# Performance work log

Measured on AMD Instinct MI355X. Metric: run time of the kernel, lower is better.

## Reference

```python
import jax, jax.numpy as jnp
import numpy as np
import math

HIDDEN = 1024
NUM_HEADS = 16
HEAD_DIM = HIDDEN // NUM_HEADS


def _rope_tables(seq_len, dim, dtype):
    inv_freq = 1.0 / (10000.0 ** (np.arange(0, dim, 2, dtype=np.float32) / dim))
    t = np.arange(seq_len, dtype=np.float32)
    freqs = np.einsum('i,j->ij', t, inv_freq)          # [S, dim/2]
    emb = np.concatenate([freqs, freqs], axis=-1)      # [S, dim]
    return jnp.asarray(np.cos(emb), dtype), jnp.asarray(np.sin(emb), dtype)


def _rotate_half(x):
    x1, x2 = x[..., : x.shape[-1] // 2], x[..., x.shape[-1] // 2:]
    return jnp.concatenate([-x2, x1], axis=-1)


def setup_inputs() -> dict:
    key = jax.random.key(0)
    k1, k2, k3 = jax.random.split(key, 3)
    B, S = 2, 2048
    x = jax.random.normal(k1, (B, S, HIDDEN), dtype=jnp.float32)
    attention_mask = jnp.ones((B, S), dtype=jnp.int32)
    w_qkv = jax.random.normal(k2, (HIDDEN, 3 * HIDDEN), dtype=jnp.float32) * (1.0 / math.sqrt(HIDDEN))
    w_out = jax.random.normal(k3, (HIDDEN, HIDDEN), dtype=jnp.float32) * (1.0 / math.sqrt(HIDDEN))
    return {"x": x, "attention_mask": attention_mask, "w_qkv": w_qkv, "w_out": w_out}


def reference(x, attention_mask, w_qkv, w_out):
    B, S, H = x.shape
    qkv = x @ w_qkv                                   # [B,S,3H]
    qkv = qkv.reshape(B, S, NUM_HEADS, 3 * HEAD_DIM).transpose(0, 2, 1, 3)  # [B,h,S,3d]
    q, k, v = jnp.split(qkv, 3, axis=-1)              # each [B,h,S,d]
    cos, sin = _rope_tables(S, HEAD_DIM, x.dtype)     # [S,d]
    cos = cos[None, None]
    sin = sin[None, None]
    q = q * cos + _rotate_half(q) * sin
    k = k * cos + _rotate_half(k) * sin
    scale = math.sqrt(HEAD_DIM)
    scores = jnp.einsum('bhqd,bhkd->bhqk', q, k) / scale  # [B,h,S,S]
    mask_value = jnp.finfo(scores.dtype).min
    scores = jnp.where(attention_mask[:, None, None, :] == 0, mask_value, scores)
    attn = jax.nn.softmax(scores, axis=-1)
    context = jnp.einsum('bhqk,bhkd->bhqd', attn, v)  # [B,h,S,d]
    context = context.transpose(0, 2, 1, 3).reshape(B, S, H)
    return context @ w_out
```

## Files before the change

### kernel.cpp

```cpp
#include <hip/hip_runtime.h>
#include <hip/hip_bf16.h>
#include <math.h>
#include <stdint.h>


typedef __bf16 bf16;
typedef __bf16 bf16x8 __attribute__((ext_vector_type(8)));
typedef __bf16 bf16x4 __attribute__((ext_vector_type(4)));
typedef float f32x4 __attribute__((ext_vector_type(4)));

#define AS1 __attribute__((address_space(1)))
#define AS3 __attribute__((address_space(3)))

__device__ __forceinline__ void gload_lds16(const void* g, void* l) {
  __builtin_amdgcn_global_load_lds((const AS1 void*)g, (AS3 void*)l, 16, 0, 0);
}

__device__ __forceinline__ f32x4 mfma16(bf16x8 a, bf16x8 b, f32x4 c) {
  return __builtin_amdgcn_mfma_f32_16x16x32_bf16(a, b, c, 0, 0, 0);
}

#define S_LEN 2048


__global__ void k_split_x(const float* __restrict__ x, bf16* __restrict__ xh,
                          bf16* __restrict__ xl) {
  int i = blockIdx.x * 256 + threadIdx.x;
  float4 v = ((const float4*)x)[i];
  float vv[4] = {v.x, v.y, v.z, v.w};
  bf16x4 h, l;
#pragma unroll
  for (int j = 0; j < 4; j++) {
    bf16 hb = (bf16)vv[j];
    h[j] = hb;
    l[j] = (bf16)(vv[j] - (float)hb);
  }
  ((bf16x4*)xh)[i] = h;
  ((bf16x4*)xl)[i] = l;
}

__global__ void k_wt_qkv(const float* __restrict__ w, bf16* __restrict__ bth,
                         bf16* __restrict__ btl) {
  __shared__ float t[32][33];
  int n0 = blockIdx.x * 32, k0 = blockIdx.y * 32;
  int tx = threadIdx.x & 31, ty = threadIdx.x >> 5;
#pragma unroll
  for (int i = 0; i < 4; i++)
    t[ty + 8 * i][tx] = w[(size_t)(k0 + ty + 8 * i) * 3072 + n0 + tx];
  __syncthreads();
#pragma unroll
  for (int i = 0; i < 4; i++) {
    int r = ty + 8 * i;
    float v = t[tx][r];
    size_t o = (size_t)(n0 + r) * 1024 + k0 + tx;
    bf16 hb = (bf16)v;
    bth[o] = hb;
    btl[o] = (bf16)(v - (float)hb);
  }
}

__global__ void k_wt_out(const float* __restrict__ w, bf16* __restrict__ bt) {
  __shared__ float t[32][33];
  int n0 = blockIdx.x * 32, k0 = blockIdx.y * 32;
  int tx = threadIdx.x & 31, ty = threadIdx.x >> 5;
#pragma unroll
  for (int i = 0; i < 4; i++)
    t[ty + 8 * i][tx] = w[(size_t)(k0 + ty + 8 * i) * 1024 + n0 + tx];
  __syncthreads();
#pragma unroll
  for (int i = 0; i < 4; i++) {
    int r = ty + 8 * i;
    bt[(size_t)(n0 + r) * 1024 + k0 + tx] = (bf16)t[tx][r];
  }
}

__global__ void k_rope_tables(float* __restrict__ ct, float* __restrict__ st) {
  int i = blockIdx.x * 256 + threadIdx.x;
  int s = i >> 5, j = i & 31;
  double invf = pow(10000.0, -(double)j / 32.0);
  double a = (double)s * invf;
  ct[i] = (float)cos(a);
  st[i] = (float)sin(a);
}

__global__ __launch_bounds__(256, 2) void k_gemm_qkv(
    const bf16* __restrict__ Ah, const bf16* __restrict__ Al,
    const bf16* __restrict__ Bh, const bf16* __restrict__ Bl,
    bf16* __restrict__ C) {
  const int K = 1024, N = 3072;
  __shared__ __align__(16) bf16 sAh[128 * 32];
  __shared__ __align__(16) bf16 sAl[128 * 32];
  __shared__ __align__(16) bf16 sBh[128 * 32];
  __shared__ __align__(16) bf16 sBl[128 * 32];
  int tid = threadIdx.x, lane = tid & 63, wid = tid >> 6;
  int m0 = blockIdx.x * 128, n0 = blockIdx.y * 128;
  int wm = wid >> 1, wn = wid & 1;

  f32x4 acc[4][4];
#pragma unroll
  for (int a = 0; a < 4; a++)
#pragma unroll
    for (int b = 0; b < 4; b++) acc[a][b] = (f32x4){0.f, 0.f, 0.f, 0.f};

  for (int k0 = 0; k0 < K; k0 += 32) {
#pragma unroll
    for (int p = 0; p < 2; p++) {
      int slot = p * 256 + tid;
      int row = slot >> 2, c16 = slot & 3;
      int cs = c16 ^ ((row >> 1) & 3);
      int ldsoff = (p * 256 + wid * 64) * 16;
      size_t ga = (size_t)(m0 + row) * K + k0 + cs * 8;
      size_t gb = (size_t)(n0 + row) * K + k0 + cs * 8;
      gload_lds16(Ah + ga, (char*)sAh + ldsoff);
      gload_lds16(Al + ga, (char*)sAl + ldsoff);
      gload_lds16(Bh + gb, (char*)sBh + ldsoff);
      gload_lds16(Bl + gb, (char*)sBl + ldsoff);
    }
    __syncthreads();

    bf16x8 fah[4], fal[4], fbh[4], fbl[4];
#pragma unroll
    for (int mf = 0; mf < 4; mf++) {
      int row = wm * 64 + mf * 16 + (lane & 15);
      int c16 = (lane >> 4) ^ ((row >> 1) & 3);
      int off = row * 64 + c16 * 16;
      fah[mf] = *(const bf16x8*)((const char*)sAh + off);
      fal[mf] = *(const bf16x8*)((const char*)sAl + off);
    }
#pragma unroll
    for (int nf = 0; nf < 4; nf++) {
      int row = wn * 64 + nf * 16 + (lane & 15);
      int c16 = (lane >> 4) ^ ((row >> 1) & 3);
      int off = row * 64 + c16 * 16;
      fbh[nf] = *(const bf16x8*)((const char*)sBh + off);
      fbl[nf] = *(const bf16x8*)((const char*)sBl + off);
    }
#pragma unroll
    for (int mf = 0; mf < 4; mf++)
#pragma unroll
      for (int nf = 0; nf < 4; nf++) {
        acc[mf][nf] = mfma16(fah[mf], fbh[nf], acc[mf][nf]);
        acc[mf][nf] = mfma16(fah[mf], fbl[nf], acc[mf][nf]);
        acc[mf][nf] = mfma16(fal[mf], fbh[nf], acc[mf][nf]);
      }
    __syncthreads();
  }

#pragma unroll
  for (int mf = 0; mf < 4; mf++)
#pragma unroll
    for (int nf = 0; nf < 4; nf++)
#pragma unroll
      for (int r = 0; r < 4; r++) {
        int row = m0 + wm * 64 + mf * 16 + (lane >> 4) * 4 + r;
        int col = n0 + wn * 64 + nf * 16 + (lane & 15);
        C[(size_t)row * N + col] = (bf16)acc[mf][nf][r];
      }
}

__global__ void k_rope_scatter(const bf16* __restrict__ QKV,
                               const float* __restrict__ ct,
                               const float* __restrict__ st,
                               bf16* __restrict__ Q, bf16* __restrict__ Kb,
                               bf16* __restrict__ Vt) {
  __shared__ __align__(16) bf16 vt[64 * 64];
  int sblk = blockIdx.x, bh = blockIdx.y;
  int b = bh >> 4, h = bh & 15;
  int tid = threadIdx.x;
  int r = tid >> 2, c = tid & 3;
  int s = sblk * 64 + r;
  size_t rowbase = ((size_t)(b * S_LEN + s)) * 3072 + h * 192;

  bf16x8 qlo = *(const bf16x8*)(QKV + rowbase + c * 8);
  bf16x8 qhi = *(const bf16x8*)(QKV + rowbase + c * 8 + 32);
  bf16x8 klo = *(const bf16x8*)(QKV + rowbase + 64 + c * 8);
  bf16x8 khi = *(const bf16x8*)(QKV + rowbase + 64 + c * 8 + 32);
  bf16x8 vlo = *(const bf16x8*)(QKV + rowbase + 128 + c * 8);
  bf16x8 vhi = *(const bf16x8*)(QKV + rowbase + 128 + c * 8 + 32);

  bf16x8 qol, qoh, kol, koh;
#pragma unroll
  for (int j = 0; j < 8; j++) {
    float cs = ct[s * 32 + c * 8 + j], sn = st[s * 32 + c * 8 + j];
    float q1 = (float)qlo[j], q2 = (float)qhi[j];
    qol[j] = (bf16)(q1 * cs - q2 * sn);
    qoh[j] = (bf16)(q2 * cs + q1 * sn);
    float k1 = (float)klo[j], k2 = (float)khi[j];
    kol[j] = (bf16)(k1 * cs - k2 * sn);
    koh[j] = (bf16)(k2 * cs + k1 * sn);
  }
  size_t qb = ((size_t)bh * S_LEN + s) * 64 + c * 8;
  *(bf16x8*)(Q + qb) = qol;
  *(bf16x8*)(Q + qb + 32) = qoh;
  *(bf16x8*)(Kb + qb) = kol;
  *(bf16x8*)(Kb + qb + 32) = koh;

#pragma unroll
  for (int j = 0; j < 8; j++) {
    vt[(c * 8 + j) * 64 + r] = vlo[j];
    vt[(c * 8 + 32 + j) * 64 + r] = vhi[j];
  }
  __syncthreads();
  int d = tid >> 2, cc = tid & 3;
  size_t vb = ((size_t)bh * 64 + d) * S_LEN + sblk * 64 + cc * 16;
  *(bf16x8*)(Vt + vb) = *(const bf16x8*)(vt + d * 64 + cc * 16);
  *(bf16x8*)(Vt + vb + 8) = *(const bf16x8*)(vt + d * 64 + cc * 16 + 8);
}

__global__ __launch_bounds__(256, 3) void k_attn(
    const bf16* __restrict__ Q, const bf16* __restrict__ Kb,
    const bf16* __restrict__ Vt, const int* __restrict__ mask,
    bf16* __restrict__ Ctx) {
  __shared__ __align__(16) bf16 sK[128 * 64];
  __shared__ __align__(16) bf16 sV[64 * 128];
  int tid = threadIdx.x, lane = tid & 63, wid = tid >> 6;
  int g = lane >> 4, q = lane & 15;
  int qt = blockIdx.x, bh = blockIdx.y;
  int b = bh >> 4, h = bh & 15;
  int q0 = qt * 128 + wid * 32;

  bf16x8 bQ[2][2];
#pragma unroll
  for (int mf = 0; mf < 2; mf++)
#pragma unroll
    for (int ks = 0; ks < 2; ks++) {
      const bf16* p = Q + ((size_t)bh * S_LEN + q0 + mf * 16 + q) * 64 + ks * 32 + g * 8;
      bf16x8 v = *(const bf16x8*)p;
#pragma unroll
      for (int j = 0; j < 8; j++) v[j] = (bf16)((float)v[j] * 0.125f);
      bQ[mf][ks] = v;
    }

  f32x4 O[2][4];
  float mrow[2], lrow[2];
#pragma unroll
  for (int mf = 0; mf < 2; mf++) {
#pragma unroll
    for (int nd = 0; nd < 4; nd++) O[mf][nd] = (f32x4){0.f, 0.f, 0.f, 0.f};
    mrow[mf] = -3e38f;
    lrow[mf] = 0.f;
  }

  for (int kt = 0; kt < 16; kt++) {
    int k0 = kt * 128;
#pragma unroll
    for (int p = 0; p < 4; p++) {
      int slot = p * 256 + tid;
      int row = slot >> 3, c16 = slot & 7;
      int cs = c16 ^ (row & 7);
      gload_lds16(Kb + ((size_t)bh * S_LEN + k0 + row) * 64 + cs * 8,
                  (char*)sK + (p * 256 + wid * 64) * 16);
    }
#pragma unroll
    for (int p = 0; p < 4; p++) {
      int slot = p * 256 + tid;
      int row = slot >> 4, c16 = slot & 15;
      int cs = c16 ^ (row & 7);
      gload_lds16(Vt + ((size_t)bh * 64 + row) * S_LEN + k0 + cs * 8,
                  (char*)sV + (p * 256 + wid * 64) * 16);
    }
    __syncthreads();

    f32x4 sfr[2][8];
#pragma unroll
    for (int mf = 0; mf < 2; mf++)
#pragma unroll
      for (int kf = 0; kf < 8; kf++) sfr[mf][kf] = (f32x4){0.f, 0.f, 0.f, 0.f};
#pragma unroll
    for (int kf = 0; kf < 8; kf++) {
#pragma unroll
      for (int ks = 0; ks < 2; ks++) {
        int row = kf * 16 + q;
        int c16 = (ks * 4 + g) ^ (row & 7);
        bf16x8 ak = *(const bf16x8*)((const char*)sK + row * 128 + c16 * 16);
        sfr[0][kf] = mfma16(ak, bQ[0][ks], sfr[0][kf]);
        sfr[1][kf] = mfma16(ak, bQ[1][ks], sfr[1][kf]);
      }
    }
#pragma unroll
    for (int kf = 0; kf < 8; kf++) {
      int4 mv = *(const int4*)(mask + b * S_LEN + k0 + kf * 16 + g * 4);
      int mm[4] = {mv.x, mv.y, mv.z, mv.w};
#pragma unroll
      for (int r = 0; r < 4; r++)
        if (mm[r] == 0) { sfr[0][kf][r] = -1e30f; sfr[1][kf][r] = -1e30f; }
    }
    float alpha[2];
#pragma unroll
    for (int mf = 0; mf < 2; mf++) {
      float mx = -3e38f;
#pragma unroll
      for (int kf = 0; kf < 8; kf++)
#pragma unroll
        for (int r = 0; r < 4; r++) mx = fmaxf(mx, sfr[mf][kf][r]);
      mx = fmaxf(mx, __shfl_xor(mx, 16, 64));
      mx = fmaxf(mx, __shfl_xor(mx, 32, 64));
      float mnew = fmaxf(mrow[mf], mx);
      float al = __expf(mrow[mf] - mnew);
      mrow[mf] = mnew;
      float ps = 0.f;
#pragma unroll
      for (int kf = 0; kf < 8; kf++)
#pragma unroll
        for (int r = 0; r < 4; r++) {
          float p0 = __expf(sfr[mf][kf][r] - mnew);
          sfr[mf][kf][r] = p0;
          ps += p0;
        }
      ps += __shfl_xor(ps, 16, 64);
      ps += __shfl_xor(ps, 32, 64);
      lrow[mf] = lrow[mf] * al + ps;
      alpha[mf] = al;
    }
#pragma unroll
    for (int mf = 0; mf < 2; mf++)
#pragma unroll
      for (int nd = 0; nd < 4; nd++)
#pragma unroll
        for (int r = 0; r < 4; r++) O[mf][nd][r] *= alpha[mf];

#pragma unroll
    for (int ks = 0; ks < 4; ks++) {
      bf16x8 pb[2];
#pragma unroll
      for (int mf = 0; mf < 2; mf++)
#pragma unroll
        for (int j = 0; j < 8; j++)
          pb[mf][j] = (bf16)sfr[mf][2 * ks + (j >> 2)][j & 3];
#pragma unroll
      for (int nd = 0; nd < 4; nd++) {
        int row = nd * 16 + q;
        int sw = (row & 7) << 4;
        bf16x4 v0 = *(const bf16x4*)((const char*)sV + row * 256 + ((ks * 64 + g * 8) ^ sw));
        bf16x4 v1 = *(const bf16x4*)((const char*)sV + row * 256 + ((ks * 64 + g * 8 + 32) ^ sw));
        bf16x8 av;
#pragma unroll
        for (int j = 0; j < 4; j++) { av[j] = v0[j]; av[4 + j] = v1[j]; }
#pragma unroll
        for (int mf = 0; mf < 2; mf++) O[mf][nd] = mfma16(av, pb[mf], O[mf][nd]);
      }
    }
    __syncthreads();
  }

#pragma unroll
  for (int mf = 0; mf < 2; mf++) {
    float inv = 1.f / lrow[mf];
    int srow = q0 + mf * 16 + q;
#pragma unroll
    for (int nd = 0; nd < 4; nd++) {
      bf16x4 o4;
#pragma unroll
      for (int r = 0; r < 4; r++) o4[r] = (bf16)(O[mf][nd][r] * inv);
      *(bf16x4*)(Ctx + ((size_t)b * S_LEN + srow) * 1024 + h * 64 + nd * 16 + g * 4) = o4;
    }
  }
}

__global__ __launch_bounds__(256, 2) void k_gemm_out(
    const bf16* __restrict__ A, const bf16* __restrict__ Bt,
    float* __restrict__ C) {
  const int K = 1024, N = 1024;
  __shared__ __align__(16) bf16 sA[128 * 32];
  __shared__ __align__(16) bf16 sB[128 * 32];
  int tid = threadIdx.x, lane = tid & 63, wid = tid >> 6;
  int m0 = blockIdx.x * 128, n0 = blockIdx.y * 128;
  int wm = wid >> 1, wn = wid & 1;

  f32x4 acc[4][4];
#pragma unroll
  for (int a = 0; a < 4; a++)
#pragma unroll
    for (int b = 0; b < 4; b++) acc[a][b] = (f32x4){0.f, 0.f, 0.f, 0.f};

  for (int k0 = 0; k0 < K; k0 += 32) {
#pragma unroll
    for (int p = 0; p < 2; p++) {
      int slot = p * 256 + tid;
      int row = slot >> 2, c16 = slot & 3;
      int cs = c16 ^ ((row >> 1) & 3);
      int ldsoff = (p * 256 + wid * 64) * 16;
      gload_lds16(A + (size_t)(m0 + row) * K + k0 + cs * 8, (char*)sA + ldsoff);
      gload_lds16(Bt + (size_t)(n0 + row) * K + k0 + cs * 8, (char*)sB + ldsoff);
    }
    __syncthreads();
    bf16x8 fa[4], fb[4];
#pragma unroll
    for (int mf = 0; mf < 4; mf++) {
      int row = wm * 64 + mf * 16 + (lane & 15);
      int c16 = (lane >> 4) ^ ((row >> 1) & 3);
      fa[mf] = *(const bf16x8*)((const char*)sA + row * 64 + c16 * 16);
    }
#pragma unroll
    for (int nf = 0; nf < 4; nf++) {
      int row = wn * 64 + nf * 16 + (lane & 15);
      int c16 = (lane >> 4) ^ ((row >> 1) & 3);
      fb[nf] = *(const bf16x8*)((const char*)sB + row * 64 + c16 * 16);
    }
#pragma unroll
    for (int mf = 0; mf < 4; mf++)
#pragma unroll
      for (int nf = 0; nf < 4; nf++)
        acc[mf][nf] = mfma16(fa[mf], fb[nf], acc[mf][nf]);
    __syncthreads();
  }
#pragma unroll
  for (int mf = 0; mf < 4; mf++)
#pragma unroll
    for (int nf = 0; nf < 4; nf++)
#pragma unroll
      for (int r = 0; r < 4; r++) {
        int row = m0 + wm * 64 + mf * 16 + (lane >> 4) * 4 + r;
        int col = n0 + wn * 64 + nf * 16 + (lane & 15);
        C[(size_t)row * N + col] = acc[mf][nf][r];
      }
}

extern "C" void kernel_launch(void* const* d_in, const int* in_sizes, int n_in,
                              void* d_out, int out_size, void* d_ws, size_t ws_size,
                              hipStream_t stream) {
  const float* x = (const float*)d_in[0];
  const int* mask = (const int*)d_in[1];
  const float* wqkv = (const float*)d_in[2];
  const float* wout = (const float*)d_in[3];
  float* out = (float*)d_out;
  char* ws = (char*)d_ws;

  bf16* Xh  = (bf16*)(ws + 0);
  bf16* Xl  = (bf16*)(ws + 8388608);
  bf16* Wqh = (bf16*)(ws + 16777216);
  bf16* Wql = (bf16*)(ws + 23068672);
  bf16* Wo  = (bf16*)(ws + 29360128);
  bf16* QKV = (bf16*)(ws + 31457280);
  bf16* Qb  = (bf16*)(ws + 56623104);
  bf16* Kb  = (bf16*)(ws + 65011712);
  bf16* Vt  = (bf16*)(ws + 73400320);
  bf16* Ctx = (bf16*)(ws + 81788928);
  float* ct = (float*)(ws + 90177536);
  float* st = (float*)(ws + 90439680);

  k_split_x<<<4096, 256, 0, stream>>>(x, Xh, Xl);
  k_wt_qkv<<<dim3(96, 32), 256, 0, stream>>>(wqkv, Wqh, Wql);
  k_wt_out<<<dim3(32, 32), 256, 0, stream>>>(wout, Wo);
  k_rope_tables<<<256, 256, 0, stream>>>(ct, st);
  k_gemm_qkv<<<dim3(32, 24), 256, 0, stream>>>(Xh, Xl, Wqh, Wql, QKV);
  k_rope_scatter<<<dim3(32, 32), 256, 0, stream>>>(QKV, ct, st, Qb, Kb, Vt);
  k_attn<<<dim3(16, 32), 256, 0, stream>>>(Qb, Kb, Vt, mask, Ctx);
  k_gemm_out<<<dim3(32, 8), 256, 0, stream>>>(Ctx, Wo, out);
}
```

Before: 265.3 us.

## Split attention keys across two wave groups with double-buffered K and merge

The attention kernel now runs 512 threads per block. Two groups of four waves each handle half of the key range, and their partial softmax states are merged through LDS at the end (split-K flash attention). K tiles are double-buffered in LDS, V is read straight from global memory instead of staged, and Q is prescaled by log2(e)/sqrt(d) in the rope kernel so exp2 can replace exp. It also skips the mask pass when a whole tile is unmasked and skips output rescaling unless the running max grows by more than 8 (lazy rescale). In exchange, V reads from global may be less coalesced, and the 64KB LDS arena limits occupancy.

```diff
diff --git a/kernel.cpp b/kernel.cpp
--- a/kernel.cpp
+++ b/kernel.cpp
@@ -21,6 +21,7 @@
 }
 
 #define S_LEN 2048
+#define QSCALE 0.1803368801111144f
 
 
 __global__ void k_split_x(const float* __restrict__ x, bf16* __restrict__ xh,
@@ -183,8 +184,8 @@
   for (int j = 0; j < 8; j++) {
     float cs = ct[s * 32 + c * 8 + j], sn = st[s * 32 + c * 8 + j];
     float q1 = (float)qlo[j], q2 = (float)qhi[j];
-    qol[j] = (bf16)(q1 * cs - q2 * sn);
-    qoh[j] = (bf16)(q2 * cs + q1 * sn);
+    qol[j] = (bf16)((q1 * cs - q2 * sn) * QSCALE);
+    qoh[j] = (bf16)((q2 * cs + q1 * sn) * QSCALE);
     float k1 = (float)klo[j], k2 = (float)khi[j];
     kol[j] = (bf16)(k1 * cs - k2 * sn);
     koh[j] = (bf16)(k2 * cs + k1 * sn);
@@ -207,29 +208,25 @@
   *(bf16x8*)(Vt + vb + 8) = *(const bf16x8*)(vt + d * 64 + cc * 16 + 8);
 }
 
-__global__ __launch_bounds__(256, 3) void k_attn(
+__global__ __launch_bounds__(512, 4) void k_attn(
     const bf16* __restrict__ Q, const bf16* __restrict__ Kb,
     const bf16* __restrict__ Vt, const int* __restrict__ mask,
     bf16* __restrict__ Ctx) {
-  __shared__ __align__(16) bf16 sK[128 * 64];
-  __shared__ __align__(16) bf16 sV[64 * 128];
-  int tid = threadIdx.x, lane = tid & 63, wid = tid >> 6;
+  __shared__ __align__(16) char arena[65536];
+  int tid = threadIdx.x, lane = tid & 63, w = tid >> 6;
+  int grp = w >> 2, wq = w & 3;
   int g = lane >> 4, q = lane & 15;
   int qt = blockIdx.x, bh = blockIdx.y;
   int b = bh >> 4, h = bh & 15;
-  int q0 = qt * 128 + wid * 32;
+  int q0 = qt * 128 + wq * 32;
 
   bf16x8 bQ[2][2];
 #pragma unroll
   for (int mf = 0; mf < 2; mf++)
 #pragma unroll
-    for (int ks = 0; ks < 2; ks++) {
-      const bf16* p = Q + ((size_t)bh * S_LEN + q0 + mf * 16 + q) * 64 + ks * 32 + g * 8;
-      bf16x8 v = *(const bf16x8*)p;
-#pragma unroll
-      for (int j = 0; j < 8; j++) v[j] = (bf16)((float)v[j] * 0.125f);
-      bQ[mf][ks] = v;
-    }
+    for (int ks = 0; ks < 2; ks++)
+      bQ[mf][ks] = *(const bf16x8*)(Q + ((size_t)bh * S_LEN + q0 + mf * 16 + q) * 64 +
+                                    ks * 32 + g * 8);
 
   f32x4 O[2][4];
   float mrow[2], lrow[2];
@@ -241,25 +238,35 @@
     lrow[mf] = 0.f;
   }
 
-  for (int kt = 0; kt < 16; kt++) {
-    int k0 = kt * 128;
-#pragma unroll
-    for (int p = 0; p < 4; p++) {
-      int slot = p * 256 + tid;
-      int row = slot >> 3, c16 = slot & 7;
-      int cs = c16 ^ (row & 7);
-      gload_lds16(Kb + ((size_t)bh * S_LEN + k0 + row) * 64 + cs * 8,
-                  (char*)sK + (p * 256 + wid * 64) * 16);
-    }
-#pragma unroll
-    for (int p = 0; p < 4; p++) {
-      int slot = p * 256 + tid;
-      int row = slot >> 4, c16 = slot & 15;
-      int cs = c16 ^ (row & 7);
-      gload_lds16(Vt + ((size_t)bh * 64 + row) * S_LEN + k0 + cs * 8,
-                  (char*)sV + (p * 256 + wid * 64) * 16);
-    }
-    __syncthreads();
+  const bf16* kbase = Kb + (size_t)bh * S_LEN * 64;
+  const bf16* vbase = Vt + (size_t)bh * 64 * S_LEN;
+  int db = 0;
+
+#pragma unroll
+  for (int p = 0; p < 4; p++) {
+    int slot = p * 512 + tid;
+    int sg = slot >> 10, within = slot & 1023;
+    int row = within >> 3, c16 = within & 7;
+    int cs = c16 ^ (row & 7);
+    gload_lds16(kbase + (size_t)(sg * 1024 + row) * 64 + cs * 8,
+                arena + slot * 16);
+  }
+  __syncthreads();
+
+  for (int kt = 0; kt < 8; kt++) {
+    int k0 = grp * 1024 + kt * 128;
+    if (kt < 7) {
+#pragma unroll
+      for (int p = 0; p < 4; p++) {
+        int slot = p * 512 + tid;
+        int sg = slot >> 10, within = slot & 1023;
+        int row = within >> 3, c16 = within & 7;
+        int cs = c16 ^ (row & 7);
+        gload_lds16(kbase + (size_t)(sg * 1024 + (kt + 1) * 128 + row) * 64 + cs * 8,
+                    arena + (db ^ 1) * 32768 + slot * 16);
+      }
+    }
+    const char* kt_lds = arena + db * 32768 + grp * 16384;
 
     f32x4 sfr[2][8];
 #pragma unroll
@@ -272,20 +279,24 @@
       for (int ks = 0; ks < 2; ks++) {
         int row = kf * 16 + q;
         int c16 = (ks * 4 + g) ^ (row & 7);
-        bf16x8 ak = *(const bf16x8*)((const char*)sK + row * 128 + c16 * 16);
+        bf16x8 ak = *(const bf16x8*)(kt_lds + row * 128 + c16 * 16);
         sfr[0][kf] = mfma16(ak, bQ[0][ks], sfr[0][kf]);
         sfr[1][kf] = mfma16(ak, bQ[1][ks], sfr[1][kf]);
       }
     }
-#pragma unroll
-    for (int kf = 0; kf < 8; kf++) {
-      int4 mv = *(const int4*)(mask + b * S_LEN + k0 + kf * 16 + g * 4);
-      int mm[4] = {mv.x, mv.y, mv.z, mv.w};
-#pragma unroll
-      for (int r = 0; r < 4; r++)
-        if (mm[r] == 0) { sfr[0][kf][r] = -1e30f; sfr[1][kf][r] = -1e30f; }
-    }
-    float alpha[2];
+    {
+      int2 mv = *(const int2*)(mask + b * S_LEN + k0 + lane * 2);
+      if (!__all(mv.x & mv.y)) {
+#pragma unroll
+        for (int kf = 0; kf < 8; kf++) {
+          int4 m4 = *(const int4*)(mask + b * S_LEN + k0 + kf * 16 + g * 4);
+          int mm[4] = {m4.x, m4.y, m4.z, m4.w};
+#pragma unroll
+          for (int r = 0; r < 4; r++)
+            if (mm[r] == 0) { sfr[0][kf][r] = -1e30f; sfr[1][kf][r] = -1e30f; }
+        }
+      }
+    }
 #pragma unroll
     for (int mf = 0; mf < 2; mf++) {
       float mx = -3e38f;
@@ -295,29 +306,29 @@
         for (int r = 0; r < 4; r++) mx = fmaxf(mx, sfr[mf][kf][r]);
       mx = fmaxf(mx, __shfl_xor(mx, 16, 64));
       mx = fmaxf(mx, __shfl_xor(mx, 32, 64));
-      float mnew = fmaxf(mrow[mf], mx);
-      float al = __expf(mrow[mf] - mnew);
-      mrow[mf] = mnew;
+      if (__any(mx > mrow[mf] + 8.0f)) {
+        float mnew = fmaxf(mrow[mf], mx);
+        float al = exp2f(mrow[mf] - mnew);
+        mrow[mf] = mnew;
+        lrow[mf] *= al;
+#pragma unroll
+        for (int nd = 0; nd < 4; nd++)
+#pragma unroll
+          for (int r = 0; r < 4; r++) O[mf][nd][r] *= al;
+      }
       float ps = 0.f;
 #pragma unroll
       for (int kf = 0; kf < 8; kf++)
 #pragma unroll
         for (int r = 0; r < 4; r++) {
-          float p0 = __expf(sfr[mf][kf][r] - mnew);
+          float p0 = exp2f(sfr[mf][kf][r] - mrow[mf]);
           sfr[mf][kf][r] = p0;
           ps += p0;
         }
       ps += __shfl_xor(ps, 16, 64);
       ps += __shfl_xor(ps, 32, 64);
-      lrow[mf] = lrow[mf] * al + ps;
-      alpha[mf] = al;
-    }
-#pragma unroll
-    for (int mf = 0; mf < 2; mf++)
-#pragma unroll
-      for (int nd = 0; nd < 4; nd++)
-#pragma unroll
-        for (int r = 0; r < 4; r++) O[mf][nd][r] *= alpha[mf];
+      lrow[mf] += ps;
+    }
 
 #pragma unroll
     for (int ks = 0; ks < 4; ks++) {
@@ -329,10 +340,9 @@
           pb[mf][j] = (bf16)sfr[mf][2 * ks + (j >> 2)][j & 3];
 #pragma unroll
       for (int nd = 0; nd < 4; nd++) {
-        int row = nd * 16 + q;
-        int sw = (row & 7) << 4;
-        bf16x4 v0 = *(const bf16x4*)((const char*)sV + row * 256 + ((ks * 64 + g * 8) ^ sw));
-        bf16x4 v1 = *(const bf16x4*)((const char*)sV + row * 256 + ((ks * 64 + g * 8 + 32) ^ sw));
+        const bf16* vrow = vbase + (size_t)(nd * 16 + q) * S_LEN + k0 + ks * 32;
+        bf16x4 v0 = *(const bf16x4*)(vrow + g * 4);
+        bf16x4 v1 = *(const bf16x4*)(vrow + 16 + g * 4);
         bf16x8 av;
 #pragma unroll
         for (int j = 0; j < 4; j++) { av[j] = v0[j]; av[4 + j] = v1[j]; }
@@ -341,18 +351,43 @@
       }
     }
     __syncthreads();
-  }
-
-#pragma unroll
-  for (int mf = 0; mf < 2; mf++) {
-    float inv = 1.f / lrow[mf];
-    int srow = q0 + mf * 16 + q;
-#pragma unroll
-    for (int nd = 0; nd < 4; nd++) {
-      bf16x4 o4;
-#pragma unroll
-      for (int r = 0; r < 4; r++) o4[r] = (bf16)(O[mf][nd][r] * inv);
-      *(bf16x4*)(Ctx + ((size_t)b * S_LEN + srow) * 1024 + h * 64 + nd * 16 + g * 4) = o4;
+    db ^= 1;
+  }
+
+  float* mO = (float*)arena;
+  float2* mML = (float2*)(arena + 33280);
+  if (grp == 1) {
+#pragma unroll
+    for (int mf = 0; mf < 2; mf++) {
+      int row = wq * 32 + mf * 16 + q;
+      if (g == 0) mML[row] = make_float2(mrow[mf], lrow[mf]);
+#pragma unroll
+      for (int nd = 0; nd < 4; nd++)
+#pragma unroll
+        for (int r = 0; r < 4; r++)
+          mO[row * 65 + nd * 16 + g * 4 + r] = O[mf][nd][r];
+    }
+  }
+  __syncthreads();
+  if (grp == 0) {
+#pragma unroll
+    for (int mf = 0; mf < 2; mf++) {
+      int row = wq * 32 + mf * 16 + q;
+      float2 ml2 = mML[row];
+      float m = fmaxf(mrow[mf], ml2.x);
+      float fA = exp2f(mrow[mf] - m), fB = exp2f(ml2.x - m);
+      float inv = 1.f / (lrow[mf] * fA + ml2.y * fB);
+      int srow = q0 + mf * 16 + q;
+#pragma unroll
+      for (int nd = 0; nd < 4; nd++) {
+        bf16x4 o4;
+#pragma unroll
+        for (int r = 0; r < 4; r++) {
+          float ob = mO[row * 65 + nd * 16 + g * 4 + r];
+          o4[r] = (bf16)((O[mf][nd][r] * fA + ob * fB) * inv);
+        }
+        *(bf16x4*)(Ctx + ((size_t)b * S_LEN + srow) * 1024 + h * 64 + nd * 16 + g * 4) = o4;
+      }
     }
   }
 }
@@ -445,6 +480,6 @@
   k_rope_tables<<<256, 256, 0, stream>>>(ct, st);
   k_gemm_qkv<<<dim3(32, 24), 256, 0, stream>>>(Xh, Xl, Wqh, Wql, QKV);
   k_rope_scatter<<<dim3(32, 32), 256, 0, stream>>>(QKV, ct, st, Qb, Kb, Vt);
-  k_attn<<<dim3(16, 32), 256, 0, stream>>>(Qb, Kb, Vt, mask, Ctx);
+  k_attn<<<dim3(16, 32), 512, 0, stream>>>(Qb, Kb, Vt, mask, Ctx);
   k_gemm_out<<<dim3(32, 8), 256, 0, stream>>>(Ctx, Wo, out);
 }
```

Result: slower. 370.6 us (+39.7%).

## Restructure attention kernel: double-buffered K, direct V reads, lazy rescale, exp2

Applied to the files above, without the earlier changes.

The attention kernel now gives each wave 16 query rows instead of 32 and launches twice as many blocks, ordered by head first. K tiles are double-buffered in LDS so the next tile's load overlaps compute, while V is read straight from global memory rather than staged in LDS. The softmax scale and log2(e) are folded into Q during the RoPE pass so exp2f can be used. Output rescaling is skipped unless the running max rises by more than 8, and mask handling is skipped when a wave sees no masked keys. Reading V from global memory avoids the LDS staging but may raise L2 traffic, and each K tile loaded into LDS is now shared by only 64 query rows instead of 128.

```diff
diff --git a/kernel.cpp b/kernel.cpp
--- a/kernel.cpp
+++ b/kernel.cpp
@@ -21,6 +21,7 @@
 }
 
 #define S_LEN 2048
+#define QSCALE 0.1803368801111144f
 
 
 __global__ void k_split_x(const float* __restrict__ x, bf16* __restrict__ xh,
@@ -183,8 +184,8 @@
   for (int j = 0; j < 8; j++) {
     float cs = ct[s * 32 + c * 8 + j], sn = st[s * 32 + c * 8 + j];
     float q1 = (float)qlo[j], q2 = (float)qhi[j];
-    qol[j] = (bf16)(q1 * cs - q2 * sn);
-    qoh[j] = (bf16)(q2 * cs + q1 * sn);
+    qol[j] = (bf16)((q1 * cs - q2 * sn) * QSCALE);
+    qoh[j] = (bf16)((q2 * cs + q1 * sn) * QSCALE);
     float k1 = (float)klo[j], k2 = (float)khi[j];
     kol[j] = (bf16)(k1 * cs - k2 * sn);
     koh[j] = (bf16)(k2 * cs + k1 * sn);
@@ -207,153 +208,141 @@
   *(bf16x8*)(Vt + vb + 8) = *(const bf16x8*)(vt + d * 64 + cc * 16 + 8);
 }
 
-__global__ __launch_bounds__(256, 3) void k_attn(
+__global__ __launch_bounds__(256, 4) void k_attn(
     const bf16* __restrict__ Q, const bf16* __restrict__ Kb,
     const bf16* __restrict__ Vt, const int* __restrict__ mask,
     bf16* __restrict__ Ctx) {
-  __shared__ __align__(16) bf16 sK[128 * 64];
-  __shared__ __align__(16) bf16 sV[64 * 128];
-  int tid = threadIdx.x, lane = tid & 63, wid = tid >> 6;
+  __shared__ __align__(16) char sK[2][16384];
+  int tid = threadIdx.x, lane = tid & 63, w = tid >> 6;
   int g = lane >> 4, q = lane & 15;
-  int qt = blockIdx.x, bh = blockIdx.y;
+  int bh = blockIdx.x, qt = blockIdx.y;
   int b = bh >> 4, h = bh & 15;
-  int q0 = qt * 128 + wid * 32;
-
-  bf16x8 bQ[2][2];
-#pragma unroll
-  for (int mf = 0; mf < 2; mf++)
-#pragma unroll
-    for (int ks = 0; ks < 2; ks++) {
-      const bf16* p = Q + ((size_t)bh * S_LEN + q0 + mf * 16 + q) * 64 + ks * 32 + g * 8;
-      bf16x8 v = *(const bf16x8*)p;
-#pragma unroll
-      for (int j = 0; j < 8; j++) v[j] = (bf16)((float)v[j] * 0.125f);
-      bQ[mf][ks] = v;
-    }
-
-  f32x4 O[2][4];
-  float mrow[2], lrow[2];
-#pragma unroll
-  for (int mf = 0; mf < 2; mf++) {
-#pragma unroll
-    for (int nd = 0; nd < 4; nd++) O[mf][nd] = (f32x4){0.f, 0.f, 0.f, 0.f};
-    mrow[mf] = -3e38f;
-    lrow[mf] = 0.f;
-  }
+  int qrow = qt * 64 + w * 16 + q;
+
+  bf16x8 bQ[2];
+#pragma unroll
+  for (int ks = 0; ks < 2; ks++)
+    bQ[ks] = *(const bf16x8*)(Q + ((size_t)bh * S_LEN + qrow) * 64 + ks * 32 + g * 8);
+
+  f32x4 O[4];
+#pragma unroll
+  for (int nd = 0; nd < 4; nd++) O[nd] = (f32x4){0.f, 0.f, 0.f, 0.f};
+  float mrow = -3e38f, lrow = 0.f;
+
+  const bf16* kbase = Kb + (size_t)bh * S_LEN * 64;
+  const bf16* vbase = Vt + (size_t)bh * 64 * S_LEN;
+  int db = 0;
+
+#pragma unroll
+  for (int p = 0; p < 4; p++) {
+    int slot = p * 256 + tid;
+    int row = slot >> 3, c16 = slot & 7;
+    int cs = c16 ^ (row & 7);
+    gload_lds16(kbase + (size_t)row * 64 + cs * 8,
+                sK[0] + (p * 256 + w * 64) * 16);
+  }
+  __syncthreads();
 
   for (int kt = 0; kt < 16; kt++) {
     int k0 = kt * 128;
-#pragma unroll
-    for (int p = 0; p < 4; p++) {
-      int slot = p * 256 + tid;
-      int row = slot >> 3, c16 = slot & 7;
-      int cs = c16 ^ (row & 7);
-      gload_lds16(Kb + ((size_t)bh * S_LEN + k0 + row) * 64 + cs * 8,
-                  (char*)sK + (p * 256 + wid * 64) * 16);
-    }
-#pragma unroll
-    for (int p = 0; p < 4; p++) {
-      int slot = p * 256 + tid;
-      int row = slot >> 4, c16 = slot & 15;
-      int cs = c16 ^ (row & 7);
-      gload_lds16(Vt + ((size_t)bh * 64 + row) * S_LEN + k0 + cs * 8,
-                  (char*)sV + (p * 256 + wid * 64) * 16);
-    }
-    __syncthreads();
-
-    f32x4 sfr[2][8];
-#pragma unroll
-    for (int mf = 0; mf < 2; mf++)
-#pragma unroll
-      for (int kf = 0; kf < 8; kf++) sfr[mf][kf] = (f32x4){0.f, 0.f, 0.f, 0.f};
+    if (kt < 15) {
+#pragma unroll
+      for (int p = 0; p < 4; p++) {
+        int slot = p * 256 + tid;
+        int row = slot >> 3, c16 = slot & 7;
+        int cs = c16 ^ (row & 7);
+        gload_lds16(kbase + (size_t)((kt + 1) * 128 + row) * 64 + cs * 8,
+                    sK[db ^ 1] + (p * 256 + w * 64) * 16);
+      }
+    }
+    const char* kl = sK[db];
+
+    f32x4 sfr[8];
+#pragma unroll
+    for (int kf = 0; kf < 8; kf++) sfr[kf] = (f32x4){0.f, 0.f, 0.f, 0.f};
 #pragma unroll
     for (int kf = 0; kf < 8; kf++) {
 #pragma unroll
       for (int ks = 0; ks < 2; ks++) {
         int row = kf * 16 + q;
         int c16 = (ks * 4 + g) ^ (row & 7);
-        bf16x8 ak = *(const bf16x8*)((const char*)sK + row * 128 + c16 * 16);
-        sfr[0][kf] = mfma16(ak, bQ[0][ks], sfr[0][kf]);
-        sfr[1][kf] = mfma16(ak, bQ[1][ks], sfr[1][kf]);
-      }
-    }
-#pragma unroll
-    for (int kf = 0; kf < 8; kf++) {
-      int4 mv = *(const int4*)(mask + b * S_LEN + k0 + kf * 16 + g * 4);
-      int mm[4] = {mv.x, mv.y, mv.z, mv.w};
-#pragma unroll
-      for (int r = 0; r < 4; r++)
-        if (mm[r] == 0) { sfr[0][kf][r] = -1e30f; sfr[1][kf][r] = -1e30f; }
-    }
-    float alpha[2];
-#pragma unroll
-    for (int mf = 0; mf < 2; mf++) {
+        bf16x8 ak = *(const bf16x8*)(kl + row * 128 + c16 * 16);
+        sfr[kf] = mfma16(ak, bQ[ks], sfr[kf]);
+      }
+    }
+    {
+      int2 mv = *(const int2*)(mask + b * S_LEN + k0 + lane * 2);
+      if (!__all(mv.x & mv.y)) {
+#pragma unroll
+        for (int kf = 0; kf < 8; kf++) {
+          int4 m4 = *(const int4*)(mask + b * S_LEN + k0 + kf * 16 + g * 4);
+          int mm[4] = {m4.x, m4.y, m4.z, m4.w};
+#pragma unroll
+          for (int r = 0; r < 4; r++)
+            if (mm[r] == 0) sfr[kf][r] = -1e30f;
+        }
+      }
+    }
+    {
       float mx = -3e38f;
 #pragma unroll
       for (int kf = 0; kf < 8; kf++)
 #pragma unroll
-        for (int r = 0; r < 4; r++) mx = fmaxf(mx, sfr[mf][kf][r]);
+        for (int r = 0; r < 4; r++) mx = fmaxf(mx, sfr[kf][r]);
       mx = fmaxf(mx, __shfl_xor(mx, 16, 64));
       mx = fmaxf(mx, __shfl_xor(mx, 32, 64));
-      float mnew = fmaxf(mrow[mf], mx);
-      float al = __expf(mrow[mf] - mnew);
-      mrow[mf] = mnew;
+      if (__any(mx > mrow + 8.0f)) {
+        float mnew = fmaxf(mrow, mx);
+        float al = exp2f(mrow - mnew);
+        mrow = mnew;
+        lrow *= al;
+#pragma unroll
+        for (int nd = 0; nd < 4; nd++)
+#pragma unroll
+          for (int r = 0; r < 4; r++) O[nd][r] *= al;
+      }
       float ps = 0.f;
 #pragma unroll
       for (int kf = 0; kf < 8; kf++)
 #pragma unroll
         for (int r = 0; r < 4; r++) {
-          float p0 = __expf(sfr[mf][kf][r] - mnew);
-          sfr[mf][kf][r] = p0;
+          float p0 = exp2f(sfr[kf][r] - mrow);
+          sfr[kf][r] = p0;
           ps += p0;
         }
       ps += __shfl_xor(ps, 16, 64);
       ps += __shfl_xor(ps, 32, 64);
-      lrow[mf] = lrow[mf] * al + ps;
-      alpha[mf] = al;
-    }
-#pragma unroll
-    for (int mf = 0; mf < 2; mf++)
-#pragma unroll
-      for (int nd = 0; nd < 4; nd++)
-#pragma unroll
-        for (int r = 0; r < 4; r++) O[mf][nd][r] *= alpha[mf];
+      lrow += ps;
+    }
 
 #pragma unroll
     for (int ks = 0; ks < 4; ks++) {
-      bf16x8 pb[2];
-#pragma unroll
-      for (int mf = 0; mf < 2; mf++)
-#pragma unroll
-        for (int j = 0; j < 8; j++)
-          pb[mf][j] = (bf16)sfr[mf][2 * ks + (j >> 2)][j & 3];
+      bf16x8 pb;
+#pragma unroll
+      for (int j = 0; j < 8; j++)
+        pb[j] = (bf16)sfr[2 * ks + (j >> 2)][j & 3];
 #pragma unroll
       for (int nd = 0; nd < 4; nd++) {
-        int row = nd * 16 + q;
-        int sw = (row & 7) << 4;
-        bf16x4 v0 = *(const bf16x4*)((const char*)sV + row * 256 + ((ks * 64 + g * 8) ^ sw));
-        bf16x4 v1 = *(const bf16x4*)((const char*)sV + row * 256 + ((ks * 64 + g * 8 + 32) ^ sw));
+        const bf16* vrow = vbase + (size_t)(nd * 16 + q) * S_LEN + k0 + ks * 32;
+        bf16x4 v0 = *(const bf16x4*)(vrow + g * 4);
+        bf16x4 v1 = *(const bf16x4*)(vrow + 16 + g * 4);
         bf16x8 av;
 #pragma unroll
         for (int j = 0; j < 4; j++) { av[j] = v0[j]; av[4 + j] = v1[j]; }
-#pragma unroll
-        for (int mf = 0; mf < 2; mf++) O[mf][nd] = mfma16(av, pb[mf], O[mf][nd]);
+        O[nd] = mfma16(av, pb, O[nd]);
       }
     }
     __syncthreads();
-  }
-
-#pragma unroll
-  for (int mf = 0; mf < 2; mf++) {
-    float inv = 1.f / lrow[mf];
-    int srow = q0 + mf * 16 + q;
-#pragma unroll
-    for (int nd = 0; nd < 4; nd++) {
-      bf16x4 o4;
-#pragma unroll
-      for (int r = 0; r < 4; r++) o4[r] = (bf16)(O[mf][nd][r] * inv);
-      *(bf16x4*)(Ctx + ((size_t)b * S_LEN + srow) * 1024 + h * 64 + nd * 16 + g * 4) = o4;
-    }
+    db ^= 1;
+  }
+
+  float inv = 1.f / lrow;
+#pragma unroll
+  for (int nd = 0; nd < 4; nd++) {
+    bf16x4 o4;
+#pragma unroll
+    for (int r = 0; r < 4; r++) o4[r] = (bf16)(O[nd][r] * inv);
+    *(bf16x4*)(Ctx + ((size_t)b * S_LEN + qrow) * 1024 + h * 64 + nd * 16 + g * 4) = o4;
   }
 }
 
@@ -445,6 +434,6 @@
   k_rope_tables<<<256, 256, 0, stream>>>(ct, st);
   k_gemm_qkv<<<dim3(32, 24), 256, 0, stream>>>(Xh, Xl, Wqh, Wql, QKV);
   k_rope_scatter<<<dim3(32, 32), 256, 0, stream>>>(QKV, ct, st, Qb, Kb, Vt);
-  k_attn<<<dim3(16, 32), 256, 0, stream>>>(Qb, Kb, Vt, mask, Ctx);
+  k_attn<<<dim3(32, 32), 256, 0, stream>>>(Qb, Kb, Vt, mask, Ctx);
   k_gemm_out<<<dim3(32, 8), 256, 0, stream>>>(Ctx, Wo, out);
 }
```

Result: slower. 420.7 us (+58.6%).
